# Optimization experiments

Measured on AMD Instinct MI355X. Metric: run time of the kernel, lower is better.

## Reference

```python
import jax, jax.numpy as jnp
import numpy as np

WIN = 11
SIGMA = 1.5
K1, K2 = 0.01, 0.03
DATA_RANGE = 1.0


def _gauss1d(size, sigma):
    coords = jnp.arange(size, dtype=jnp.float32) - size // 2
    g = jnp.exp(-(coords ** 2) / (2.0 * sigma ** 2))
    return g / g.sum()


def _blur(x, g):
    # Separable depthwise Gaussian blur, VALID padding, matching F.conv2d(groups=C).
    C = x.shape[1]
    w = g.astype(x.dtype)
    kh = jnp.broadcast_to(w.reshape(1, 1, WIN, 1), (C, 1, WIN, 1))  # blur along H
    kw = jnp.broadcast_to(w.reshape(1, 1, 1, WIN), (C, 1, 1, WIN))  # blur along W
    dn = ('NCHW', 'OIHW', 'NCHW')
    out = jax.lax.conv_general_dilated(x, kh, (1, 1), 'VALID',
                                       dimension_numbers=dn, feature_group_count=C)
    out = jax.lax.conv_general_dilated(out, kw, (1, 1), 'VALID',
                                       dimension_numbers=dn, feature_group_count=C)
    return out


def setup_inputs() -> dict:
    key = jax.random.key(0)
    k1, k2 = jax.random.split(key)
    shape = (16, 3, 512, 512)
    image1 = jax.random.uniform(k1, shape, dtype=jnp.float32)
    image2 = jax.random.uniform(k2, shape, dtype=jnp.float32)
    window = _gauss1d(WIN, SIGMA)
    return {"image1": image1, "image2": image2, "window": window}


def reference(image1, image2, window):
    c1 = (K1 * DATA_RANGE) ** 2
    c2 = (K2 * DATA_RANGE) ** 2
    mu1 = _blur(image1, window)
    mu2 = _blur(image2, window)
    mu1_sq = mu1 * mu1
    mu2_sq = mu2 * mu2
    mu1_mu2 = mu1 * mu2
    sigma1_sq = _blur(image1 * image1, window) - mu1_sq
    sigma2_sq = _blur(image2 * image2, window) - mu2_sq
    sigma12 = _blur(image1 * image2, window) - mu1_mu2
    cs_map = (2.0 * sigma12 + c2) / (sigma1_sq + sigma2_sq + c2)
    ssim_map = (2.0 * mu1_mu2 + c1) / (mu1_sq + mu2_sq + c1) * cs_map
    # flatten(2).mean(-1) then .mean() over (B,C) == full mean (uniform sizes)
    return ssim_map.mean()
```

## Files before the change

kernel.cpp:

```cpp
#include <hip/hip_runtime.h>

#define WIN   11
#define IW    512
#define IH    512
#define OW    502
#define OH    502
#define NCH   48
#define TW    54
#define SWC   64
#define SWP4  67
#define CH    8
#define NCHUNK 4
#define SLABH (CH*NCHUNK)
#define NGX   10
#define NGY   16
#define PXL   7

typedef float v2f __attribute__((ext_vector_type(2)));
typedef float v4f __attribute__((ext_vector_type(4)));

__device__ __forceinline__ float fast_rcp(float x) {
    return __builtin_amdgcn_rcpf(x);
}

template<bool EDGE>
__device__ __forceinline__ void ssim_slab(const float* __restrict__ p1,
                                          const float* __restrict__ p2,
                                          const float (&w)[WIN],
                                          v4f (*vb)[SWP4],
                                          int x0, int y0, int tid, float& acc)
{
    const int c = tid;
    int gx = x0 + c;
    if (EDGE) gx = min(gx, IW - 1);

    v2f h[10];
#pragma unroll
    for (int j = 0; j < 10; ++j) {
        int gy = y0 + j; if (EDGE) gy = min(gy, IH - 1);
        const int gidx = gy * IW + gx;
        h[j].x = p1[gidx];
        h[j].y = p2[gidx];
    }

    const int rh = tid & 7;
    const int gg = tid >> 3;
    const int xs = gg * PXL;
    const float c1 = 0.0001f;
    const float c2 = 0.0009f;

#pragma unroll
    for (int ci = 0; ci < NCHUNK; ++ci) {
        const int jbase = y0 + 10 + ci * CH;
        v2f n[CH];
#pragma unroll
        for (int j = 0; j < CH; ++j) {
            int gy = jbase + j; if (EDGE) gy = min(gy, IH - 1);
            const int gidx = gy * IW + gx;
            n[j].x = p1[gidx];
            n[j].y = p2[gidx];
        }

        v2f accA[CH], accB[CH];
#pragma unroll
        for (int r = 0; r < CH; ++r) {
            accA[r] = (v2f){0.f, 0.f};
            accB[r] = (v2f){0.f, 0.f};
        }
#pragma unroll
        for (int j = 0; j < CH + 10; ++j) {
            v2f ab = (j < 10) ? h[j] : n[j - 10];
            v2f st;
            st.x = fmaf(ab.x, ab.x, ab.y * ab.y);
            st.y = ab.x * ab.y;
#pragma unroll
            for (int k = 0; k < WIN; ++k) {
                const int r = j - k;
                if (r >= 0 && r < CH) {
                    v2f ws; ws.x = w[k]; ws.y = w[k];
                    accA[r] = __builtin_elementwise_fma(ws, ab, accA[r]);
                    accB[r] = __builtin_elementwise_fma(ws, st, accB[r]);
                }
            }
            if (j >= 10) {
                v4f o4;
                o4.x = accA[j - 10].x; o4.y = accA[j - 10].y;
                o4.z = accB[j - 10].x; o4.w = accB[j - 10].y;
                vb[j - 10][c] = o4;
            }
        }
#pragma unroll
        for (int j = 0; j < 10; ++j)
            h[j] = (j < 2) ? h[8 + j] : n[j - 2];

        __syncthreads();

        {
            v4f x4[17];
            const v4f* src = &vb[rh][xs];
#pragma unroll
            for (int t = 0; t < 17; ++t)
                x4[t] = src[t];

            const int oy = y0 + ci * CH + rh;
#pragma unroll
            for (int o = 0; o < PXL; ++o) {
                v2f sA = {0.f, 0.f}, sB = {0.f, 0.f};
#pragma unroll
                for (int k = 0; k < WIN; ++k) {
                    v4f f = x4[o + k];
                    v2f lo = __builtin_shufflevector(f, f, 0, 1);
                    v2f hi = __builtin_shufflevector(f, f, 2, 3);
                    v2f ws; ws.x = w[k]; ws.y = w[k];
                    sA = __builtin_elementwise_fma(ws, lo, sA);
                    sB = __builtin_elementwise_fma(ws, hi, sB);
                }
                const int tc = xs + o;
                bool valid = (tc < TW);
                if (EDGE) valid = valid && (oy < OH) && ((x0 + tc) < OW);
                if (valid) {
                    float m1 = sA.x, m2 = sA.y;
                    float mu11 = m1 * m1, mu22 = m2 * m2, mu12 = m1 * m2;
                    float sAB = sB.x - mu11 - mu22;
                    float s12 = sB.y - mu12;
                    float num = (2.f * mu12 + c1) * (2.f * s12 + c2);
                    float den = (mu11 + mu22 + c1) * (sAB + c2);
                    acc += num * fast_rcp(den);
                }
            }
        }
        __syncthreads();
    }
}

__global__ __launch_bounds__(64, 2)
void ssim_fused_kernel(const float* __restrict__ img1,
                       const float* __restrict__ img2,
                       const float* __restrict__ win,
                       float* __restrict__ partial)
{
    __shared__ __align__(16) v4f vbuf[CH][SWP4];
    const int tid = threadIdx.x;
    const int ch = blockIdx.z;
    const int x0 = blockIdx.x * TW;
    const int y0 = blockIdx.y * SLABH;
    const float* __restrict__ p1 = img1 + (size_t)ch * (IW * IH);
    const float* __restrict__ p2 = img2 + (size_t)ch * (IW * IH);

    float w[WIN];
#pragma unroll
    for (int k = 0; k < WIN; ++k) w[k] = win[k];

    float acc = 0.f;
    const bool edge = (blockIdx.x == gridDim.x - 1) || (blockIdx.y == gridDim.y - 1);
    if (edge) ssim_slab<true >(p1, p2, w, vbuf, x0, y0, tid, acc);
    else      ssim_slab<false>(p1, p2, w, vbuf, x0, y0, tid, acc);

#pragma unroll
    for (int off = 32; off > 0; off >>= 1)
        acc += __shfl_down(acc, off, 64);
    if (tid == 0) {
        partial[(size_t)blockIdx.z * (gridDim.x * gridDim.y)
                + blockIdx.y * gridDim.x + blockIdx.x] = acc;
    }
}

__global__ __launch_bounds__(256)
void reduce_partials_kernel(const float* __restrict__ partial, int n4,
                            float* __restrict__ out, double inv_count)
{
    __shared__ double sd[256];
    const float4* p4 = reinterpret_cast<const float4*>(partial);
    double s = 0.0;
    for (int i = threadIdx.x; i < n4; i += 256) {
        float4 f = p4[i];
        s += (double)f.x + (double)f.y + (double)f.z + (double)f.w;
    }
    sd[threadIdx.x] = s;
    __syncthreads();
    for (int off = 128; off > 0; off >>= 1) {
        if (threadIdx.x < off) sd[threadIdx.x] += sd[threadIdx.x + off];
        __syncthreads();
    }
    if (threadIdx.x == 0)
        out[0] = (float)(sd[0] * inv_count);
}

extern "C" void kernel_launch(void* const* d_in, const int* in_sizes, int n_in,
                              void* d_out, int out_size, void* d_ws, size_t ws_size,
                              hipStream_t stream)
{
    const float* img1 = (const float*)d_in[0];
    const float* img2 = (const float*)d_in[1];
    const float* win  = (const float*)d_in[2];
    float* out = (float*)d_out;
    float* partial = (float*)d_ws;

    dim3 grid(NGX, NGY, NCH);
    dim3 block(64);

    ssim_fused_kernel<<<grid, block, 0, stream>>>(img1, img2, win, partial);

    const int nblocks = NGX * NGY * NCH;
    const double inv_count = 1.0 / ((double)NCH * OW * OH);
    reduce_partials_kernel<<<1, 256, 0, stream>>>(partial, nblocks / 4, out, inv_count);
}
```

Baseline: 49.17 us.

## Pack four channels per block with per-wave LDS and drop barriers

Each 256-thread block now processes four channels, one wavefront per channel, each with its own LDS staging buffer. Because every buffer is private to a single wavefront, both __syncthreads calls are removed, relying on in-order LDS access within a wave. The LDS row pitch drops from 67 to 64 entries, and the last lane group's two out-of-range reads are guarded. The aims are to cut barrier cost and per-block launch overhead. The risks are more LDS bank conflicts from the unpadded pitch, and correctness resting on compiler and hardware ordering without explicit synchronisation.

Measured after the change: 49.34 us. Within noise of the previous version (+0.4%).

```diff
diff --git a/kernel.cpp b/kernel.cpp
--- a/kernel.cpp
+++ b/kernel.cpp
@@ -8,12 +8,13 @@
 #define NCH   48
 #define TW    54
 #define SWC   64
-#define SWP4  67
+#define SWP4  64
 #define CH    8
 #define NCHUNK 4
 #define SLABH (CH*NCHUNK)
 #define NGX   10
 #define NGY   16
+#define NGZ   12
 #define PXL   7
 
 typedef float v2f __attribute__((ext_vector_type(2)));
@@ -28,9 +29,9 @@
                                           const float* __restrict__ p2,
                                           const float (&w)[WIN],
                                           v4f (*vb)[SWP4],
-                                          int x0, int y0, int tid, float& acc)
-{
-    const int c = tid;
+                                          int x0, int y0, int lane, float& acc)
+{
+    const int c = lane;
     int gx = x0 + c;
     if (EDGE) gx = min(gx, IW - 1);
 
@@ -43,8 +44,8 @@
         h[j].y = p2[gidx];
     }
 
-    const int rh = tid & 7;
-    const int gg = tid >> 3;
+    const int rh = lane & 7;
+    const int gg = lane >> 3;
     const int xs = gg * PXL;
     const float c1 = 0.0001f;
     const float c2 = 0.0009f;
@@ -93,14 +94,15 @@
         for (int j = 0; j < 10; ++j)
             h[j] = (j < 2) ? h[8 + j] : n[j - 2];
 
-        __syncthreads();
-
         {
             v4f x4[17];
             const v4f* src = &vb[rh][xs];
 #pragma unroll
-            for (int t = 0; t < 17; ++t)
+            for (int t = 0; t < 15; ++t)
                 x4[t] = src[t];
+            if (gg < 7) { x4[15] = src[15]; x4[16] = src[16]; }
+            else        { x4[15] = (v4f){0.f,0.f,0.f,0.f};
+                          x4[16] = (v4f){0.f,0.f,0.f,0.f}; }
 
             const int oy = y0 + ci * CH + rh;
 #pragma unroll
@@ -129,19 +131,20 @@
                 }
             }
         }
-        __syncthreads();
-    }
-}
-
-__global__ __launch_bounds__(64, 2)
+    }
+}
+
+__global__ __launch_bounds__(256, 2)
 void ssim_fused_kernel(const float* __restrict__ img1,
                        const float* __restrict__ img2,
                        const float* __restrict__ win,
                        float* __restrict__ partial)
 {
-    __shared__ __align__(16) v4f vbuf[CH][SWP4];
-    const int tid = threadIdx.x;
-    const int ch = blockIdx.z;
+    __shared__ __align__(16) v4f vbuf[4][CH][SWP4];
+    const int tid  = threadIdx.x;
+    const int wid  = tid >> 6;
+    const int lane = tid & 63;
+    const int ch   = blockIdx.z * 4 + wid;
     const int x0 = blockIdx.x * TW;
     const int y0 = blockIdx.y * SLABH;
     const float* __restrict__ p1 = img1 + (size_t)ch * (IW * IH);
@@ -153,15 +156,14 @@
 
     float acc = 0.f;
     const bool edge = (blockIdx.x == gridDim.x - 1) || (blockIdx.y == gridDim.y - 1);
-    if (edge) ssim_slab<true >(p1, p2, w, vbuf, x0, y0, tid, acc);
-    else      ssim_slab<false>(p1, p2, w, vbuf, x0, y0, tid, acc);
+    if (edge) ssim_slab<true >(p1, p2, w, vbuf[wid], x0, y0, lane, acc);
+    else      ssim_slab<false>(p1, p2, w, vbuf[wid], x0, y0, lane, acc);
 
 #pragma unroll
     for (int off = 32; off > 0; off >>= 1)
         acc += __shfl_down(acc, off, 64);
-    if (tid == 0) {
-        partial[(size_t)blockIdx.z * (gridDim.x * gridDim.y)
-                + blockIdx.y * gridDim.x + blockIdx.x] = acc;
+    if (lane == 0) {
+        partial[(size_t)ch * (NGX * NGY) + blockIdx.y * NGX + blockIdx.x] = acc;
     }
 }
 
@@ -196,8 +198,8 @@
     float* out = (float*)d_out;
     float* partial = (float*)d_ws;
 
-    dim3 grid(NGX, NGY, NCH);
-    dim3 block(64);
+    dim3 grid(NGX, NGY, NGZ);
+    dim3 block(256);
 
     ssim_fused_kernel<<<grid, block, 0, stream>>>(img1, img2, win, partial);
 
```

## Software-pipeline vertical and horizontal passes with double-buffered LDS and row prefetch

Applied to the files above, without the earlier changes.

Unrolls the four row chunks by hand into a software pipeline. It alternates two LDS buffers and prefetches the next chunk's global rows while the current vertical pass runs. The horizontal pass for chunk i now interleaves with the vertical pass for chunk i+1, and the __syncthreads barriers are dropped. That relies on the 64-thread block being a single wavefront, so LDS ordering holds within the wave. The cost is more live registers (two row buffers plus the x4 staging array) and double the LDS footprint.

After: 52.51 us. 1.07x slower.

```diff
diff --git a/kernel.cpp b/kernel.cpp
--- a/kernel.cpp
+++ b/kernel.cpp
@@ -24,10 +24,103 @@
 }
 
 template<bool EDGE>
+__device__ __forceinline__ void load_rows(const float* __restrict__ p1,
+                                          const float* __restrict__ p2,
+                                          int gx, int jbase, v2f (&dst)[CH])
+{
+#pragma unroll
+    for (int j = 0; j < CH; ++j) {
+        int gy = jbase + j; if (EDGE) gy = min(gy, IH - 1);
+        const int gidx = gy * IW + gx;
+        dst[j].x = p1[gidx];
+        dst[j].y = p2[gidx];
+    }
+}
+
+__device__ __forceinline__ void vpass(const float (&w)[WIN],
+                                      v2f (&h)[10], const v2f (&cur)[CH],
+                                      v4f (*vb)[SWP4], int c)
+{
+    v2f accA[CH], accB[CH];
+#pragma unroll
+    for (int r = 0; r < CH; ++r) {
+        accA[r] = (v2f){0.f, 0.f};
+        accB[r] = (v2f){0.f, 0.f};
+    }
+#pragma unroll
+    for (int j = 0; j < CH + 10; ++j) {
+        v2f ab = (j < 10) ? h[j] : cur[j - 10];
+        v2f st;
+        st.x = fmaf(ab.x, ab.x, ab.y * ab.y);
+        st.y = ab.x * ab.y;
+#pragma unroll
+        for (int k = 0; k < WIN; ++k) {
+            const int r = j - k;
+            if (r >= 0 && r < CH) {
+                v2f ws; ws.x = w[k]; ws.y = w[k];
+                accA[r] = __builtin_elementwise_fma(ws, ab, accA[r]);
+                accB[r] = __builtin_elementwise_fma(ws, st, accB[r]);
+            }
+        }
+        if (j >= 10) {
+            v4f o4;
+            o4.x = accA[j - 10].x; o4.y = accA[j - 10].y;
+            o4.z = accB[j - 10].x; o4.w = accB[j - 10].y;
+            vb[j - 10][c] = o4;
+        }
+    }
+#pragma unroll
+    for (int j = 0; j < 10; ++j)
+        h[j] = (j < 2) ? h[8 + j] : cur[j - 2];
+}
+
+__device__ __forceinline__ void hissue(const v4f (*vb)[SWP4], int rh, int xs,
+                                       v4f (&x4)[17])
+{
+    const v4f* src = &vb[rh][xs];
+#pragma unroll
+    for (int t = 0; t < 17; ++t)
+        x4[t] = src[t];
+}
+
+template<bool EDGE>
+__device__ __forceinline__ void hcompute(const v4f (&x4)[17], const float (&w)[WIN],
+                                         int oy, int x0, int xs, float& acc)
+{
+    const float c1 = 0.0001f;
+    const float c2 = 0.0009f;
+#pragma unroll
+    for (int o = 0; o < PXL; ++o) {
+        v2f sA = {0.f, 0.f}, sB = {0.f, 0.f};
+#pragma unroll
+        for (int k = 0; k < WIN; ++k) {
+            v4f f = x4[o + k];
+            v2f lo = __builtin_shufflevector(f, f, 0, 1);
+            v2f hi = __builtin_shufflevector(f, f, 2, 3);
+            v2f ws; ws.x = w[k]; ws.y = w[k];
+            sA = __builtin_elementwise_fma(ws, lo, sA);
+            sB = __builtin_elementwise_fma(ws, hi, sB);
+        }
+        const int tc = xs + o;
+        bool valid = (tc < TW);
+        if (EDGE) valid = valid && (oy < OH) && ((x0 + tc) < OW);
+        if (valid) {
+            float m1 = sA.x, m2 = sA.y;
+            float mu11 = m1 * m1, mu22 = m2 * m2, mu12 = m1 * m2;
+            float sAB = sB.x - mu11 - mu22;
+            float s12 = sB.y - mu12;
+            float num = (2.f * mu12 + c1) * (2.f * s12 + c2);
+            float den = (mu11 + mu22 + c1) * (sAB + c2);
+            acc += num * fast_rcp(den);
+        }
+    }
+}
+
+template<bool EDGE>
 __device__ __forceinline__ void ssim_slab(const float* __restrict__ p1,
                                           const float* __restrict__ p2,
                                           const float (&w)[WIN],
-                                          v4f (*vb)[SWP4],
+                                          v4f (*buf0)[SWP4], v4f (*buf1)[SWP4],
                                           int x0, int y0, int tid, float& acc)
 {
     const int c = tid;
@@ -42,95 +135,34 @@
         h[j].x = p1[gidx];
         h[j].y = p2[gidx];
     }
+    v2f nA[CH], nB[CH];
+    load_rows<EDGE>(p1, p2, gx, y0 + 10, nA);
 
     const int rh = tid & 7;
     const int gg = tid >> 3;
     const int xs = gg * PXL;
-    const float c1 = 0.0001f;
-    const float c2 = 0.0009f;
-
-#pragma unroll
-    for (int ci = 0; ci < NCHUNK; ++ci) {
-        const int jbase = y0 + 10 + ci * CH;
-        v2f n[CH];
-#pragma unroll
-        for (int j = 0; j < CH; ++j) {
-            int gy = jbase + j; if (EDGE) gy = min(gy, IH - 1);
-            const int gidx = gy * IW + gx;
-            n[j].x = p1[gidx];
-            n[j].y = p2[gidx];
-        }
-
-        v2f accA[CH], accB[CH];
-#pragma unroll
-        for (int r = 0; r < CH; ++r) {
-            accA[r] = (v2f){0.f, 0.f};
-            accB[r] = (v2f){0.f, 0.f};
-        }
-#pragma unroll
-        for (int j = 0; j < CH + 10; ++j) {
-            v2f ab = (j < 10) ? h[j] : n[j - 10];
-            v2f st;
-            st.x = fmaf(ab.x, ab.x, ab.y * ab.y);
-            st.y = ab.x * ab.y;
-#pragma unroll
-            for (int k = 0; k < WIN; ++k) {
-                const int r = j - k;
-                if (r >= 0 && r < CH) {
-                    v2f ws; ws.x = w[k]; ws.y = w[k];
-                    accA[r] = __builtin_elementwise_fma(ws, ab, accA[r]);
-                    accB[r] = __builtin_elementwise_fma(ws, st, accB[r]);
-                }
-            }
-            if (j >= 10) {
-                v4f o4;
-                o4.x = accA[j - 10].x; o4.y = accA[j - 10].y;
-                o4.z = accB[j - 10].x; o4.w = accB[j - 10].y;
-                vb[j - 10][c] = o4;
-            }
-        }
-#pragma unroll
-        for (int j = 0; j < 10; ++j)
-            h[j] = (j < 2) ? h[8 + j] : n[j - 2];
-
-        __syncthreads();
-
-        {
-            v4f x4[17];
-            const v4f* src = &vb[rh][xs];
-#pragma unroll
-            for (int t = 0; t < 17; ++t)
-                x4[t] = src[t];
-
-            const int oy = y0 + ci * CH + rh;
-#pragma unroll
-            for (int o = 0; o < PXL; ++o) {
-                v2f sA = {0.f, 0.f}, sB = {0.f, 0.f};
-#pragma unroll
-                for (int k = 0; k < WIN; ++k) {
-                    v4f f = x4[o + k];
-                    v2f lo = __builtin_shufflevector(f, f, 0, 1);
-                    v2f hi = __builtin_shufflevector(f, f, 2, 3);
-                    v2f ws; ws.x = w[k]; ws.y = w[k];
-                    sA = __builtin_elementwise_fma(ws, lo, sA);
-                    sB = __builtin_elementwise_fma(ws, hi, sB);
-                }
-                const int tc = xs + o;
-                bool valid = (tc < TW);
-                if (EDGE) valid = valid && (oy < OH) && ((x0 + tc) < OW);
-                if (valid) {
-                    float m1 = sA.x, m2 = sA.y;
-                    float mu11 = m1 * m1, mu22 = m2 * m2, mu12 = m1 * m2;
-                    float sAB = sB.x - mu11 - mu22;
-                    float s12 = sB.y - mu12;
-                    float num = (2.f * mu12 + c1) * (2.f * s12 + c2);
-                    float den = (mu11 + mu22 + c1) * (sAB + c2);
-                    acc += num * fast_rcp(den);
-                }
-            }
-        }
-        __syncthreads();
-    }
+
+    vpass(w, h, nA, buf0, c);
+    load_rows<EDGE>(p1, p2, gx, y0 + 18, nB);
+
+    v4f x4[17];
+
+    hissue(buf0, rh, xs, x4);
+    vpass(w, h, nB, buf1, c);
+    load_rows<EDGE>(p1, p2, gx, y0 + 26, nA);
+    hcompute<EDGE>(x4, w, y0 + 0 * CH + rh, x0, xs, acc);
+
+    hissue(buf1, rh, xs, x4);
+    vpass(w, h, nA, buf0, c);
+    load_rows<EDGE>(p1, p2, gx, y0 + 34, nB);
+    hcompute<EDGE>(x4, w, y0 + 1 * CH + rh, x0, xs, acc);
+
+    hissue(buf0, rh, xs, x4);
+    vpass(w, h, nB, buf1, c);
+    hcompute<EDGE>(x4, w, y0 + 2 * CH + rh, x0, xs, acc);
+
+    hissue(buf1, rh, xs, x4);
+    hcompute<EDGE>(x4, w, y0 + 3 * CH + rh, x0, xs, acc);
 }
 
 __global__ __launch_bounds__(64, 2)
@@ -139,7 +171,7 @@
                        const float* __restrict__ win,
                        float* __restrict__ partial)
 {
-    __shared__ __align__(16) v4f vbuf[CH][SWP4];
+    __shared__ __align__(16) v4f vbuf[2][CH][SWP4];
     const int tid = threadIdx.x;
     const int ch = blockIdx.z;
     const int x0 = blockIdx.x * TW;
@@ -153,8 +185,8 @@
 
     float acc = 0.f;
     const bool edge = (blockIdx.x == gridDim.x - 1) || (blockIdx.y == gridDim.y - 1);
-    if (edge) ssim_slab<true >(p1, p2, w, vbuf, x0, y0, tid, acc);
-    else      ssim_slab<false>(p1, p2, w, vbuf, x0, y0, tid, acc);
+    if (edge) ssim_slab<true >(p1, p2, w, vbuf[0], vbuf[1], x0, y0, tid, acc);
+    else      ssim_slab<false>(p1, p2, w, vbuf[0], vbuf[1], x0, y0, tid, acc);
 
 #pragma unroll
     for (int off = 32; off > 0; off >>= 1)
```
